# Kernel tuning notes

Measured on AMD Instinct MI355X. Metric: run time of the kernel, lower is better.

The kernel has to match this reference:

```python
import jax, jax.numpy as jnp
import numpy as np

B, T, D, H, O = 1024, 256, 63, 128, 14


def _lstm_dir(x, W_ih, W_hh, b_ih, b_hh):
    """Single-direction LSTM over x [B,T,D] -> hidden outputs [B,T,H].
    PyTorch gate order: i, f, g, o."""
    # Precompute input projection for all timesteps (one big GEMM).
    xp = x @ W_ih.T + (b_ih + b_hh)  # [B,T,4H]

    def step(carry, xt):
        h, c = carry
        gates = xt + h @ W_hh.T  # [B,4H]
        i, f, g, o = jnp.split(gates, 4, axis=-1)
        i = jax.nn.sigmoid(i)
        f = jax.nn.sigmoid(f)
        g = jnp.tanh(g)
        o = jax.nn.sigmoid(o)
        c = f * c + i * g
        h = o * jnp.tanh(c)
        return (h, c), h

    h0 = jnp.zeros((x.shape[0], W_hh.shape[1]), x.dtype)
    (_, _), hs = jax.lax.scan(step, (h0, h0), jnp.swapaxes(xp, 0, 1))
    return jnp.swapaxes(hs, 0, 1)  # [B,T,H]


def setup_inputs() -> dict:
    key = jax.random.key(0)
    ks = jax.random.split(key, 11)
    s = 1.0 / np.sqrt(H)  # PyTorch LSTM init scale
    return {
        "x": jax.random.normal(ks[0], (B, T, D), jnp.float32),
        "W_ih_f": jax.random.uniform(ks[1], (4 * H, D), jnp.float32, -s, s),
        "W_hh_f": jax.random.uniform(ks[2], (4 * H, H), jnp.float32, -s, s),
        "b_ih_f": jax.random.uniform(ks[3], (4 * H,), jnp.float32, -s, s),
        "b_hh_f": jax.random.uniform(ks[4], (4 * H,), jnp.float32, -s, s),
        "W_ih_b": jax.random.uniform(ks[5], (4 * H, D), jnp.float32, -s, s),
        "W_hh_b": jax.random.uniform(ks[6], (4 * H, H), jnp.float32, -s, s),
        "b_ih_b": jax.random.uniform(ks[7], (4 * H,), jnp.float32, -s, s),
        "b_hh_b": jax.random.uniform(ks[8], (4 * H,), jnp.float32, -s, s),
        "W_fc": jax.random.uniform(ks[9], (O, 2 * H), jnp.float32, -s, s),
        "b_fc": jax.random.uniform(ks[10], (O,), jnp.float32, -s, s),
    }


def reference(x, W_ih_f, W_hh_f, b_ih_f, b_hh_f,
              W_ih_b, W_hh_b, b_ih_b, b_hh_b, W_fc, b_fc):
    h_f = _lstm_dir(x, W_ih_f, W_hh_f, b_ih_f, b_hh_f)            # fwd dir
    h_b = _lstm_dir(x[:, ::-1], W_ih_b, W_hh_b, b_ih_b, b_hh_b)[:, ::-1]  # bwd dir
    # out[:, -1, :] of the BiLSTM; dropout is identity at inference.
    last = jnp.concatenate([h_f[:, -1], h_b[:, -1]], axis=-1)  # [B, 2H]
    return last @ W_fc.T + b_fc  # [B, O]
```

## Files before the change

kernel.cpp:

```cpp
#include <hip/hip_runtime.h>

typedef __attribute__((ext_vector_type(8))) short bf16x8;
typedef __attribute__((ext_vector_type(4))) float f32x4;

#define BB 1024
#define TT 256
#define DD 63
#define HH 128
#define CHUNK 4
#define HSTR 160
#define XSTR 96

#define LDS_BARRIER() asm volatile("s_waitcnt lgkmcnt(0)\n\ts_barrier" ::: "memory")

__device__ __forceinline__ short f2bf(float f) {
  unsigned u = __builtin_bit_cast(unsigned, f);
  u = (u + 0x7FFFu + ((u >> 16) & 1u)) >> 16;
  return (short)u;
}
__device__ __forceinline__ float sigm(float x) {
  return __builtin_amdgcn_rcpf(1.f + __expf(-x));
}
__device__ __forceinline__ float tanh_fast(float x) {
  float e = __expf(2.f * x);
  return 1.f - 2.f * __builtin_amdgcn_rcpf(e + 1.f);
}

__global__ __launch_bounds__(512, 2)
void lstm_fwd_kernel(const float* __restrict__ X,
                     const float* __restrict__ Wih,
                     const float* __restrict__ Whh,
                     const float* __restrict__ bih,
                     const float* __restrict__ bhh,
                     const float* __restrict__ Wfc,
                     float* __restrict__ out) {
  __shared__ __align__(16) short hbuf[2 * 4 * HSTR];
  __shared__ __align__(16) short xbuf[2 * 4 * XSTR];
  __shared__ __align__(16) float fst[4 * HH];

  const int tid  = threadIdx.x;
  const int wave = tid >> 6;
  const int lane = tid & 63;
  const int quad = lane >> 4;
  const int l15  = lane & 15;
  const int b0   = blockIdx.x * CHUNK;
  const int br   = l15 & 3;
  const int p    = l15 >> 2;

  bf16x8 Ah[4][4];
  bf16x8 Axw[4][2];
  f32x4  bias[4];
#pragma unroll
  for (int g = 0; g < 4; ++g) {
    const int n = g * 128 + wave * 16 + l15;
    const float* wr = Whh + (size_t)n * HH;
#pragma unroll
    for (int ks = 0; ks < 4; ++ks) {
      const int k0 = ks * 32 + quad * 8;
      f32x4 w0 = *(const f32x4*)(wr + k0);
      f32x4 w1 = *(const f32x4*)(wr + k0 + 4);
      bf16x8 v;
#pragma unroll
      for (int jj = 0; jj < 4; ++jj) { v[jj] = f2bf(w0[jj]); v[4 + jj] = f2bf(w1[jj]); }
      Ah[g][ks] = v;
    }
    const float* xr = Wih + (size_t)n * DD;
#pragma unroll
    for (int ks = 0; ks < 2; ++ks) {
      const int k0 = ks * 32 + quad * 8;
      bf16x8 v;
#pragma unroll
      for (int jj = 0; jj < 8; ++jj) {
        const int k = k0 + jj;
        v[jj] = (k < DD) ? f2bf(xr[k]) : (short)0;
      }
      Axw[g][ks] = v;
    }
    const int cb = g * 128 + wave * 16 + quad * 4;
    f32x4 b1 = *(const f32x4*)&bih[cb];
    f32x4 b2 = *(const f32x4*)&bhh[cb];
    bias[g] = b1 + b2;
  }

  for (int i = tid; i < 2 * 4 * HSTR; i += 512) hbuf[i] = 0;

  const int xrow = tid / DD;
  const int xd   = tid - xrow * DD;
  const bool xthr = (tid < CHUNK * DD);
  const float* xptr = X + ((size_t)(b0 + xrow) * TT) * DD + xd;
  float xv_pend = 0.f;
  if (tid >= CHUNK * DD && tid < 256) {
    const int rr = tid & 3;
    xbuf[rr * XSTR + DD] = 0;
    xbuf[4 * XSTR + rr * XSTR + DD] = 0;
  }
  if (xthr) {
    xbuf[xrow * XSTR + xd] = f2bf(xptr[0]);
    xv_pend = xptr[DD];
    xptr += 2 * DD;
  }
  __syncthreads();

  float cc = 0.f, hv = 0.f;
  const int hcol = wave * 16 + quad * 4 + p;

  for (int t = 0; t < TT; ++t) {
    const int xcur = (t & 1) * (4 * XSTR);
    const int hcur = (t & 1) * (4 * HSTR);

    float xv_new = 0.f;
    const bool pf2 = xthr && (t + 2 < TT);
    if (pf2) { xv_new = *xptr; xptr += DD; }

    bf16x8 Bh_[4], Bx_[2];
#pragma unroll
    for (int ks = 0; ks < 4; ++ks)
      Bh_[ks] = *(const bf16x8*)&hbuf[hcur + br * HSTR + ks * 32 + quad * 8];
#pragma unroll
    for (int ks = 0; ks < 2; ++ks)
      Bx_[ks] = *(const bf16x8*)&xbuf[xcur + br * XSTR + ks * 32 + quad * 8];

    f32x4 acc[4];
#pragma unroll
    for (int g = 0; g < 4; ++g)
      acc[g] = __builtin_amdgcn_mfma_f32_16x16x32_bf16(Ah[g][0], Bh_[0], bias[g], 0, 0, 0);
#pragma unroll
    for (int ks = 1; ks < 4; ++ks)
#pragma unroll
      for (int g = 0; g < 4; ++g)
        acc[g] = __builtin_amdgcn_mfma_f32_16x16x32_bf16(Ah[g][ks], Bh_[ks], acc[g], 0, 0, 0);
#pragma unroll
    for (int ks = 0; ks < 2; ++ks)
#pragma unroll
      for (int g = 0; g < 4; ++g)
        acc[g] = __builtin_amdgcn_mfma_f32_16x16x32_bf16(Axw[g][ks], Bx_[ks], acc[g], 0, 0, 0);

    const bool s0 = (l15 & 4) != 0;
    const bool s1 = (l15 & 8) != 0;
    float gv4[4];
#pragma unroll
    for (int g = 0; g < 4; ++g) {
      const float a01 = s0 ? acc[g][1] : acc[g][0];
      const float a23 = s0 ? acc[g][3] : acc[g][2];
      gv4[g] = s1 ? a23 : a01;
    }
    const float iv = sigm(gv4[0]);
    const float fv = sigm(gv4[1]);
    const float gg = tanh_fast(gv4[2]);
    const float ov = sigm(gv4[3]);
    cc = fv * cc + iv * gg;
    hv = ov * tanh_fast(cc);
    hbuf[(hcur ^ (4 * HSTR)) + br * HSTR + hcol] = f2bf(hv);

    if (xthr && (t + 1 < TT))
      xbuf[(xcur ^ (4 * XSTR)) + xrow * XSTR + xd] = f2bf(xv_pend);
    xv_pend = xv_new;
    LDS_BARRIER();
  }

  fst[br * HH + hcol] = hv;
  __syncthreads();
  if (tid < CHUNK * 14) {
    const int rr = tid / 14, o = tid - rr * 14;
    const float* wr = Wfc + (size_t)o * (2 * HH);
    float acc = 0.f;
#pragma unroll 16
    for (int k = 0; k < HH; ++k) acc += wr[k] * fst[rr * HH + k];
    out[(size_t)(b0 + rr) * 14 + o] = acc;
  }
}

__global__ __launch_bounds__(256, 2)
void lstm_bwd_fc_kernel(const float* __restrict__ X,
                        const float* __restrict__ Wih_b,
                        const float* __restrict__ bih_b,
                        const float* __restrict__ bhh_b,
                        const float* __restrict__ Wfc,
                        const float* __restrict__ bfc,
                        float* __restrict__ out) {
  __shared__ float xl[DD];
  __shared__ float glb[4 * HH];
  __shared__ float hl[HH];
  __shared__ float pl[14 * 8];
  const int b = blockIdx.x;
  const int tid = threadIdx.x;

  if (tid < DD) xl[tid] = X[((size_t)b * TT + (TT - 1)) * DD + tid];
  __syncthreads();

#pragma unroll
  for (int u = 0; u < 2; ++u) {
    const int n = tid * 2 + u;
    const float* wr = Wih_b + (size_t)n * DD;
    float acc = bih_b[n] + bhh_b[n];
#pragma unroll
    for (int k = 0; k < DD; ++k) acc += wr[k] * xl[k];
    glb[n] = acc;
  }
  __syncthreads();

  if (tid < HH) {
    float iv = sigm(glb[0 * HH + tid]);
    float gv = tanh_fast(glb[2 * HH + tid]);
    float ov = sigm(glb[3 * HH + tid]);
    hl[tid] = ov * tanh_fast(iv * gv);
  }
  __syncthreads();

  if (tid < 14 * 8) {
    const int o = tid >> 3, kp = tid & 7;
    const float* wr = Wfc + (size_t)o * (2 * HH) + HH;
    float acc = 0.f;
#pragma unroll
    for (int i = 0; i < 16; ++i) {
      const int jj = kp * 16 + i;
      acc += wr[jj] * hl[jj];
    }
    pl[tid] = acc;
  }
  __syncthreads();

  if (tid < 14) {
    float acc = bfc[tid];
#pragma unroll
    for (int i = 0; i < 8; ++i) acc += pl[tid * 8 + i];
    out[(size_t)b * 14 + tid] += acc;
  }
}

extern "C" void kernel_launch(void* const* d_in, const int* in_sizes, int n_in,
                              void* d_out, int out_size, void* d_ws, size_t ws_size,
                              hipStream_t stream) {
  const float* X     = (const float*)d_in[0];
  const float* Wih_f = (const float*)d_in[1];
  const float* Whh_f = (const float*)d_in[2];
  const float* bih_f = (const float*)d_in[3];
  const float* bhh_f = (const float*)d_in[4];
  const float* Wih_b = (const float*)d_in[5];
  const float* bih_b = (const float*)d_in[7];
  const float* bhh_b = (const float*)d_in[8];
  const float* Wfc   = (const float*)d_in[9];
  const float* bfc   = (const float*)d_in[10];
  float* out = (float*)d_out;

  lstm_fwd_kernel<<<BB / CHUNK, 512, 0, stream>>>(X, Wih_f, Whh_f, bih_f, bhh_f, Wfc, out);
  lstm_bwd_fc_kernel<<<BB, 256, 0, stream>>>(X, Wih_b, bih_b, bhh_b, Wfc, bfc, out);
}
```

Measured before the change: 303.1 us.

## Batch backward-direction kernel over 16 rows and reorder MFMA chains per gate

```diff
diff --git a/kernel.cpp b/kernel.cpp
--- a/kernel.cpp
+++ b/kernel.cpp
@@ -10,6 +10,7 @@
 #define CHUNK 4
 #define HSTR 160
 #define XSTR 96
+#define BWB 16
 
 #define LDS_BARRIER() asm volatile("s_waitcnt lgkmcnt(0)\n\ts_barrier" ::: "memory")
 
@@ -45,7 +46,6 @@
   const int l15  = lane & 15;
   const int b0   = blockIdx.x * CHUNK;
   const int br   = l15 & 3;
-  const int p    = l15 >> 2;
 
   bf16x8 Ah[4][4];
   bf16x8 Axw[4][2];
@@ -83,17 +83,17 @@
   }
 
   for (int i = tid; i < 2 * 4 * HSTR; i += 512) hbuf[i] = 0;
+  if (tid >= CHUNK * DD && tid < 256) {
+    const int rr = tid & 3;
+    xbuf[rr * XSTR + DD] = 0;
+    xbuf[4 * XSTR + rr * XSTR + DD] = 0;
+  }
 
   const int xrow = tid / DD;
   const int xd   = tid - xrow * DD;
   const bool xthr = (tid < CHUNK * DD);
   const float* xptr = X + ((size_t)(b0 + xrow) * TT) * DD + xd;
   float xv_pend = 0.f;
-  if (tid >= CHUNK * DD && tid < 256) {
-    const int rr = tid & 3;
-    xbuf[rr * XSTR + DD] = 0;
-    xbuf[4 * XSTR + rr * XSTR + DD] = 0;
-  }
   if (xthr) {
     xbuf[xrow * XSTR + xd] = f2bf(xptr[0]);
     xv_pend = xptr[DD];
@@ -102,7 +102,9 @@
   __syncthreads();
 
   float cc = 0.f, hv = 0.f;
-  const int hcol = wave * 16 + quad * 4 + p;
+  const int hcol = wave * 16 + quad * 4 + (l15 >> 2);
+  const bool s0 = (l15 & 4) != 0;
+  const bool s1 = (l15 & 8) != 0;
 
   for (int t = 0; t < TT; ++t) {
     const int xcur = (t & 1) * (4 * XSTR);
@@ -120,36 +122,23 @@
     for (int ks = 0; ks < 2; ++ks)
       Bx_[ks] = *(const bf16x8*)&xbuf[xcur + br * XSTR + ks * 32 + quad * 8];
 
-    f32x4 acc[4];
-#pragma unroll
-    for (int g = 0; g < 4; ++g)
-      acc[g] = __builtin_amdgcn_mfma_f32_16x16x32_bf16(Ah[g][0], Bh_[0], bias[g], 0, 0, 0);
-#pragma unroll
-    for (int ks = 1; ks < 4; ++ks)
-#pragma unroll
-      for (int g = 0; g < 4; ++g)
-        acc[g] = __builtin_amdgcn_mfma_f32_16x16x32_bf16(Ah[g][ks], Bh_[ks], acc[g], 0, 0, 0);
-#pragma unroll
-    for (int ks = 0; ks < 2; ++ks)
-#pragma unroll
-      for (int g = 0; g < 4; ++g)
-        acc[g] = __builtin_amdgcn_mfma_f32_16x16x32_bf16(Axw[g][ks], Bx_[ks], acc[g], 0, 0, 0);
-
-    const bool s0 = (l15 & 4) != 0;
-    const bool s1 = (l15 & 8) != 0;
-    float gv4[4];
+    float gact[4];
 #pragma unroll
     for (int g = 0; g < 4; ++g) {
-      const float a01 = s0 ? acc[g][1] : acc[g][0];
-      const float a23 = s0 ? acc[g][3] : acc[g][2];
-      gv4[g] = s1 ? a23 : a01;
-    }
-    const float iv = sigm(gv4[0]);
-    const float fv = sigm(gv4[1]);
-    const float gg = tanh_fast(gv4[2]);
-    const float ov = sigm(gv4[3]);
-    cc = fv * cc + iv * gg;
-    hv = ov * tanh_fast(cc);
+      f32x4 a = __builtin_amdgcn_mfma_f32_16x16x32_bf16(Ah[g][0], Bh_[0], bias[g], 0, 0, 0);
+      a = __builtin_amdgcn_mfma_f32_16x16x32_bf16(Ah[g][1], Bh_[1], a, 0, 0, 0);
+      a = __builtin_amdgcn_mfma_f32_16x16x32_bf16(Ah[g][2], Bh_[2], a, 0, 0, 0);
+      a = __builtin_amdgcn_mfma_f32_16x16x32_bf16(Ah[g][3], Bh_[3], a, 0, 0, 0);
+      a = __builtin_amdgcn_mfma_f32_16x16x32_bf16(Axw[g][0], Bx_[0], a, 0, 0, 0);
+      a = __builtin_amdgcn_mfma_f32_16x16x32_bf16(Axw[g][1], Bx_[1], a, 0, 0, 0);
+      const float a01 = s0 ? a[1] : a[0];
+      const float a23 = s0 ? a[3] : a[2];
+      const float v = s1 ? a23 : a01;
+      gact[g] = (g == 2) ? tanh_fast(v) : sigm(v);
+    }
+
+    cc = gact[1] * cc + gact[0] * gact[2];
+    hv = gact[3] * tanh_fast(cc);
     hbuf[(hcur ^ (4 * HSTR)) + br * HSTR + hcol] = f2bf(hv);
 
     if (xthr && (t + 1 < TT))
@@ -178,53 +167,54 @@
                         const float* __restrict__ Wfc,
                         const float* __restrict__ bfc,
                         float* __restrict__ out) {
-  __shared__ float xl[DD];
-  __shared__ float glb[4 * HH];
-  __shared__ float hl[HH];
-  __shared__ float pl[14 * 8];
-  const int b = blockIdx.x;
+  __shared__ float xl[BWB * 64];
+  __shared__ float glb[BWB * 512];
+  __shared__ float hl[BWB * HH];
   const int tid = threadIdx.x;
-
-  if (tid < DD) xl[tid] = X[((size_t)b * TT + (TT - 1)) * DD + tid];
+  const int b0  = blockIdx.x * BWB;
+
+  for (int i = tid; i < BWB * DD; i += 256) {
+    const int b = i / DD, k = i - b * DD;
+    xl[b * 64 + k] = X[((size_t)(b0 + b) * TT + (TT - 1)) * DD + k];
+  }
   __syncthreads();
 
 #pragma unroll
   for (int u = 0; u < 2; ++u) {
-    const int n = tid * 2 + u;
+    const int n = tid + u * 256;
     const float* wr = Wih_b + (size_t)n * DD;
-    float acc = bih_b[n] + bhh_b[n];
-#pragma unroll
-    for (int k = 0; k < DD; ++k) acc += wr[k] * xl[k];
-    glb[n] = acc;
-  }
-  __syncthreads();
-
-  if (tid < HH) {
-    float iv = sigm(glb[0 * HH + tid]);
-    float gv = tanh_fast(glb[2 * HH + tid]);
-    float ov = sigm(glb[3 * HH + tid]);
-    hl[tid] = ov * tanh_fast(iv * gv);
-  }
-  __syncthreads();
-
-  if (tid < 14 * 8) {
-    const int o = tid >> 3, kp = tid & 7;
+    const float bb = bih_b[n] + bhh_b[n];
+    float accs[BWB];
+#pragma unroll
+    for (int b = 0; b < BWB; ++b) accs[b] = bb;
+    for (int k = 0; k < DD; ++k) {
+      const float w = wr[k];
+#pragma unroll
+      for (int b = 0; b < BWB; ++b) accs[b] += w * xl[b * 64 + k];
+    }
+#pragma unroll
+    for (int b = 0; b < BWB; ++b) glb[b * 512 + n] = accs[b];
+  }
+  __syncthreads();
+
+#pragma unroll
+  for (int u = 0; u < 8; ++u) {
+    const int idx = tid + u * 256;
+    const int b = idx >> 7, j = idx & 127;
+    const float iv = sigm(glb[b * 512 + j]);
+    const float gv = tanh_fast(glb[b * 512 + 256 + j]);
+    const float ov = sigm(glb[b * 512 + 384 + j]);
+    hl[b * HH + j] = ov * tanh_fast(iv * gv);
+  }
+  __syncthreads();
+
+  if (tid < BWB * 14) {
+    const int b = tid / 14, o = tid - b * 14;
     const float* wr = Wfc + (size_t)o * (2 * HH) + HH;
-    float acc = 0.f;
-#pragma unroll
-    for (int i = 0; i < 16; ++i) {
-      const int jj = kp * 16 + i;
-      acc += wr[jj] * hl[jj];
-    }
-    pl[tid] = acc;
-  }
-  __syncthreads();
-
-  if (tid < 14) {
-    float acc = bfc[tid];
-#pragma unroll
-    for (int i = 0; i < 8; ++i) acc += pl[tid * 8 + i];
-    out[(size_t)b * 14 + tid] += acc;
+    float acc = bfc[o];
+#pragma unroll 16
+    for (int k = 0; k < HH; ++k) acc += wr[k] * hl[b * HH + k];
+    out[(size_t)(b0 + b) * 14 + o] += acc;
   }
 }
 
@@ -244,5 +234,5 @@
   float* out = (float*)d_out;
 
   lstm_fwd_kernel<<<BB / CHUNK, 512, 0, stream>>>(X, Wih_f, Whh_f, bih_f, bhh_f, Wfc, out);
-  lstm_bwd_fc_kernel<<<BB, 256, 0, stream>>>(X, Wih_b, bih_b, bhh_b, Wfc, bfc, out);
-}
+  lstm_bwd_fc_kernel<<<BB / BWB, 256, 0, stream>>>(X, Wih_b, bih_b, bhh_b, Wfc, bfc, out);
+}
```

Measured after the change: 285.8 us. 5.7% less time.
